# Kernel tuning notes

Hardware: AMD Instinct MI355X
Metric: run time of the kernel (lower is better)

Reference implementation:

```python
import jax, jax.numpy as jnp
import numpy as np

DIM = 256
NUM_HEADS = 8
HEAD_DIM = DIM // NUM_HEADS


def setup_inputs() -> dict:
    key = jax.random.key(0)
    k_x, k_wq, k_bq, k_wp, k_bp = jax.random.split(key, 5)
    B, C, H, W = 2, DIM, 48, 48
    x = jax.random.normal(k_x, (B, C, H, W), dtype=jnp.float32)
    # 1x1 convs are pointwise matmuls: store weights as [out, in]
    w_qkv = jax.random.normal(k_wq, (3 * C, C), dtype=jnp.float32) * (1.0 / np.sqrt(C))
    b_qkv = jax.random.normal(k_bq, (3 * C,), dtype=jnp.float32) * 0.01
    w_proj = jax.random.normal(k_wp, (C, C), dtype=jnp.float32) * (1.0 / np.sqrt(C))
    b_proj = jax.random.normal(k_bp, (C,), dtype=jnp.float32) * 0.01
    return {"x": x, "w_qkv": w_qkv, "b_qkv": b_qkv, "w_proj": w_proj, "b_proj": b_proj}


def reference(x, w_qkv, b_qkv, w_proj, b_proj):
    B, C, H, W = x.shape
    N = H * W
    # qkv 1x1 conv -> pointwise channel matmul
    qkv = jnp.einsum('bchw,oc->bohw', x, w_qkv) + b_qkv[None, :, None, None]
    q, k, v = jnp.split(qkv, 3, axis=1)  # each [B, C, H, W]
    q = q.reshape(B, NUM_HEADS, HEAD_DIM, N)
    k = k.reshape(B, NUM_HEADS, HEAD_DIM, N)
    v = v.reshape(B, NUM_HEADS, HEAD_DIM, N)
    scale = 1.0 / (HEAD_DIM ** 0.5)
    attn = jnp.einsum('bhdn,bhdm->bhnm', q, k) * scale  # [B, H, N, N]
    attn = jax.nn.softmax(attn, axis=-1)
    out = jnp.einsum('bhnm,bhdm->bhdn', attn, v)  # [B, heads, head_dim, N]
    out = out.reshape(B, C, H, W)
    out = jnp.einsum('bchw,oc->bohw', out, w_proj) + b_proj[None, :, None, None]
    return out + x
```

## Files before the change

### kernel.cpp

```cpp
#include <hip/hip_runtime.h>
#include <math.h>

#define C_DIM 256
#define NH 8
#define HD 32
#define BATCH 2
#define NPIX 2304
#define TK 64
#define NGRP (NPIX / 16)
#define TPB 18

typedef __attribute__((ext_vector_type(8))) short bf16x8;
typedef __attribute__((ext_vector_type(4))) float f32x4;

#define OFF_XT  0u
#define OFF_Q   1179648u
#define OFF_K   2359296u
#define OFF_V   3538944u
#define OFF_OT  4718592u
#define OFF_WQ  5898240u
#define OFF_WP  6094848u
#define OFF_F32 6160384u

__device__ __forceinline__ unsigned short f2b(float f) {
    union { float f; unsigned int u; } c; c.f = f;
    unsigned int u = c.u + 0x7FFFu + ((c.u >> 16) & 1u);
    return (unsigned short)(u >> 16);
}
__device__ __forceinline__ unsigned int pk2(float lo, float hi) {
    union { float f; unsigned int u; } a, b;
    a.f = lo; b.f = hi;
    return __builtin_amdgcn_perm(b.u + 0x8000u, a.u + 0x8000u, 0x07060302u);
}

__global__ __launch_bounds__(256) void prep_xt(
        const float* __restrict__ x, unsigned short* __restrict__ xT)
{
    __shared__ unsigned short t_s[64][72];
    const int tid = threadIdx.x;
    const int n0 = blockIdx.x * 64, c0 = blockIdx.y * 64, b = blockIdx.z;
    const int nl = tid & 63, cq = tid >> 6;
    #pragma unroll
    for (int p = 0; p < 8; ++p) {
        const int c = p * 8 + cq * 2;
        const float f0 = x[((size_t)b * C_DIM + c0 + c) * NPIX + n0 + nl];
        const float f1 = x[((size_t)b * C_DIM + c0 + c + 1) * NPIX + n0 + nl];
        *(unsigned int*)&t_s[nl][c] = pk2(f0, f1);
    }
    __syncthreads();
    const int row = tid >> 2, jq = tid & 3;
    #pragma unroll
    for (int hh = 0; hh < 2; ++hh) {
        const int jl = jq * 2 + hh;
        const int jg = blockIdx.y * 8 + jl;
        const int ngrp = blockIdx.x * 4 + (row >> 4);
        unsigned short* dst = xT + (((size_t)b * NGRP + ngrp) * 32 + jg) * 128 + (row & 15) * 8;
        *(uint4*)dst = *(uint4*)&t_s[row][jl * 8];
    }
}

__global__ __launch_bounds__(256) void prep_w(
        const float* __restrict__ wqkv, const float* __restrict__ wproj,
        unsigned short* __restrict__ wq, unsigned short* __restrict__ wp)
{
    const int t = blockIdx.x * 256 + threadIdx.x;
    const float* src; unsigned short* dst;
    if (t < 24576) {
        const int m = t >> 5, j = t & 31;
        src = wqkv + ((size_t)m * C_DIM + j * 8);
        dst = wq + ((size_t)((m >> 4) * 32 + j) * 16 + (m & 15)) * 8;
    } else {
        const int t2 = t - 24576, m = t2 >> 5, j = t2 & 31;
        src = wproj + ((size_t)m * C_DIM + j * 8);
        dst = wp + ((size_t)((m >> 4) * 32 + j) * 16 + (m & 15)) * 8;
    }
    const float4 f0 = *(const float4*)src, f1 = *(const float4*)(src + 4);
    *(uint4*)dst = make_uint4(pk2(f0.x, f0.y), pk2(f0.z, f0.w),
                              pk2(f1.x, f1.y), pk2(f1.z, f1.w));
}

__global__ __launch_bounds__(256, 2) void qkv_gemm(
        const unsigned short* __restrict__ xT, const unsigned short* __restrict__ wq,
        const float* __restrict__ bias,
        unsigned short* __restrict__ Qg, unsigned short* __restrict__ Kg,
        unsigned short* __restrict__ Vg)
{
    __shared__ unsigned short eplds[4][2560];
    const int tid = threadIdx.x, wv = tid >> 6, lane = tid & 63;
    const int l15 = lane & 15, quad = lane >> 4;
    const int n0 = blockIdx.x * 256, my = blockIdx.y, b = blockIdx.z;
    const int nw = n0 + wv * 64;

    bf16x8 af[2][8];
    #pragma unroll
    for (int mt = 0; mt < 2; ++mt)
        #pragma unroll
        for (int kc = 0; kc < 8; ++kc)
            af[mt][kc] = *(const bf16x8*)(wq +
                ((size_t)((my * 2 + mt) * 32 + kc * 4 + quad) * 16 + l15) * 8);

    f32x4 acc[2][4];
    #pragma unroll
    for (int mt = 0; mt < 2; ++mt)
        #pragma unroll
        for (int s = 0; s < 4; ++s) acc[mt][s] = (f32x4){0.f, 0.f, 0.f, 0.f};

    #pragma unroll
    for (int sub = 0; sub < 4; ++sub) {
        const int ngrp = (nw + sub * 16) >> 4;
        const unsigned short* bp = xT + ((size_t)b * NGRP + ngrp) * 32 * 128;
        #pragma unroll
        for (int kc = 0; kc < 8; ++kc) {
            const bf16x8 bf = *(const bf16x8*)(bp + (size_t)(kc * 4 + quad) * 128 + l15 * 8);
            acc[0][sub] = __builtin_amdgcn_mfma_f32_16x16x32_bf16(af[0][kc], bf, acc[0][sub], 0, 0, 0);
            acc[1][sub] = __builtin_amdgcn_mfma_f32_16x16x32_bf16(af[1][kc], bf, acc[1][sub], 0, 0, 0);
        }
    }

    const int which = my >> 3;
    const int h = my & 7, bh = b * NH + h;
    float4 b4[2];
    b4[0] = *(const float4*)(bias + my * 32 + quad * 4);
    b4[1] = *(const float4*)(bias + my * 32 + 16 + quad * 4);
    unsigned short* wl = eplds[wv];

    if (which < 2) {
        const float sc = (which == 0) ? 0.17677669529663687f : 1.0f;
        #pragma unroll
        for (int mt = 0; mt < 2; ++mt)
            #pragma unroll
            for (int sub = 0; sub < 4; ++sub) {
                const float v0 = (acc[mt][sub][0] + b4[mt].x) * sc;
                const float v1 = (acc[mt][sub][1] + b4[mt].y) * sc;
                const float v2 = (acc[mt][sub][2] + b4[mt].z) * sc;
                const float v3 = (acc[mt][sub][3] + b4[mt].w) * sc;
                *(uint2*)&wl[(sub * 16 + l15) * 40 + mt * 16 + quad * 4] =
                    make_uint2(pk2(v0, v1), pk2(v2, v3));
            }
        unsigned short* dst = ((which == 0) ? Qg : Kg)
                            + ((size_t)bh * NPIX + nw + lane) * HD;
        #pragma unroll
        for (int i = 0; i < 4; ++i)
            *((uint4*)dst + i) = *(uint4*)&wl[lane * 40 + i * 8];
    } else {
        #pragma unroll
        for (int mt = 0; mt < 2; ++mt)
            #pragma unroll
            for (int sub = 0; sub < 4; ++sub) {
                wl[(mt * 16 + quad * 4 + 0) * 72 + sub * 16 + l15] = f2b(acc[mt][sub][0] + b4[mt].x);
                wl[(mt * 16 + quad * 4 + 1) * 72 + sub * 16 + l15] = f2b(acc[mt][sub][1] + b4[mt].y);
                wl[(mt * 16 + quad * 4 + 2) * 72 + sub * 16 + l15] = f2b(acc[mt][sub][2] + b4[mt].z);
                wl[(mt * 16 + quad * 4 + 3) * 72 + sub * 16 + l15] = f2b(acc[mt][sub][3] + b4[mt].w);
            }
        const int row = lane >> 1, seg = (lane & 1) * 32;
        unsigned short* dst = Vg + ((size_t)bh * HD + row) * NPIX + nw + seg;
        #pragma unroll
        for (int i = 0; i < 4; ++i)
            *((uint4*)dst + i) = *(uint4*)&wl[row * 72 + seg + i * 8];
    }
}

__global__ __launch_bounds__(256, 4) void attn_kernel(
        const unsigned short* __restrict__ Qg, const unsigned short* __restrict__ Kg,
        const unsigned short* __restrict__ Vg,
        float* __restrict__ OtP, float* __restrict__ lsumP)
{
    __shared__ unsigned short k_s[2][TK][40];
    __shared__ unsigned short v_s[2][HD][76];
    __shared__ unsigned short p_s[4][16][76];

    const int tid  = threadIdx.x;
    const int wv   = tid >> 6;
    const int lane = tid & 63;
    const int l15  = lane & 15;
    const int quad = lane >> 4;
    const int bh   = blockIdx.x;
    const int q0   = blockIdx.y * 64;
    const int sp   = blockIdx.z;
    const int t0   = sp * TPB;

    const unsigned short* Qh = Qg + (size_t)bh * NPIX * HD;
    const unsigned short* Kh = Kg + (size_t)bh * NPIX * HD;
    const unsigned short* Vh = Vg + (size_t)bh * HD * NPIX;

    const bf16x8 q_frag = *(const bf16x8*)(Qh + (size_t)(q0 + wv * 16 + l15) * HD + quad * 8);

    const int kr = tid >> 2, kc = (tid & 3) * 8;
    const int vd = tid >> 3, vc = (tid & 7) * 8;

    uint4 kreg = *(const uint4*)(Kh + (size_t)(t0 * TK + kr) * HD + kc);
    uint4 vreg = *(const uint4*)(Vh + (size_t)vd * NPIX + t0 * TK + vc);
    *(uint4*)&k_s[0][kr][kc] = kreg;
    *(uint4*)&v_s[0][vd][vc] = vreg;

    f32x4 o0 = {0.f, 0.f, 0.f, 0.f};
    f32x4 o1 = {0.f, 0.f, 0.f, 0.f};
    float lsum = 0.f;

    for (int t = 0; t < TPB; ++t) {
        const int cur = t & 1;
        if (t + 1 < TPB) {
            const int k0 = (t0 + t + 1) * TK;
            kreg = *(const uint4*)(Kh + (size_t)(k0 + kr) * HD + kc);
            vreg = *(const uint4*)(Vh + (size_t)vd * NPIX + k0 + vc);
        }
        __syncthreads();

        f32x4 s[4];
        #pragma unroll
        for (int kg = 0; kg < 4; ++kg) {
            const bf16x8 kf = *(const bf16x8*)&k_s[cur][kg * 16 + l15][quad * 8];
            s[kg] = __builtin_amdgcn_mfma_f32_16x16x32_bf16(kf, q_frag,
                        (f32x4){0.f, 0.f, 0.f, 0.f}, 0, 0, 0);
        }

        #pragma unroll
        for (int kg = 0; kg < 4; ++kg) {
            const float p0 = __expf(s[kg][0]);
            const float p1 = __expf(s[kg][1]);
            const float p2 = __expf(s[kg][2]);
            const float p3 = __expf(s[kg][3]);
            lsum += (p0 + p1) + (p2 + p3);
            *(uint2*)&p_s[wv][l15][kg * 16 + quad * 4] =
                make_uint2(pk2(p0, p1), pk2(p2, p3));
        }

        #pragma unroll
        for (int kc2 = 0; kc2 < 2; ++kc2) {
            const bf16x8 pf  = *(const bf16x8*)&p_s[wv][l15][kc2 * 32 + quad * 8];
            const bf16x8 vf0 = *(const bf16x8*)&v_s[cur][l15][kc2 * 32 + quad * 8];
            const bf16x8 vf1 = *(const bf16x8*)&v_s[cur][16 + l15][kc2 * 32 + quad * 8];
            o0 = __builtin_amdgcn_mfma_f32_16x16x32_bf16(vf0, pf, o0, 0, 0, 0);
            o1 = __builtin_amdgcn_mfma_f32_16x16x32_bf16(vf1, pf, o1, 0, 0, 0);
        }

        if (t + 1 < TPB) {
            *(uint4*)&k_s[cur ^ 1][kr][kc] = kreg;
            *(uint4*)&v_s[cur ^ 1][vd][vc] = vreg;
        }
    }

    lsum += __shfl_xor(lsum, 16, 64);
    lsum += __shfl_xor(lsum, 32, 64);

    __syncthreads();
    float* pp = (float*)&p_s[wv][0][0];
    #pragma unroll
    for (int r = 0; r < 4; ++r) {
        pp[l15 * 36 + quad * 4 + r]      = o0[r];
        pp[l15 * 36 + 16 + quad * 4 + r] = o1[r];
    }
    if (quad == 0)
        lsumP[((size_t)sp * 16 + bh) * NPIX + q0 + wv * 16 + l15] = lsum;
    __syncthreads();
    const int q = lane >> 2, off = (lane & 3) * 8;
    float* dst = OtP + (((size_t)sp * 16 + bh) * NPIX + q0 + wv * 16 + q) * 32 + off;
    *(float4*)dst       = *(float4*)&pp[q * 36 + off];
    *((float4*)dst + 1) = *(float4*)&pp[q * 36 + off + 4];
}

__global__ __launch_bounds__(256) void norm_kernel(
        const float* __restrict__ OtP, const float* __restrict__ lsumP,
        unsigned short* __restrict__ OtT)
{
    const int q = blockIdx.x * 256 + threadIdx.x;
    const int bh = blockIdx.y;
    const float* pa = OtP + ((size_t)bh * NPIX + q) * 32;
    const float* pb = OtP + ((size_t)(16 + bh) * NPIX + q) * 32;
    const float inv = 1.f / (lsumP[(size_t)bh * NPIX + q] +
                             lsumP[(size_t)(16 + bh) * NPIX + q]);
    const int b = bh >> 3, h = bh & 7;
    unsigned short* cell = OtT + (((size_t)b * NGRP + (q >> 4)) * 32 + h * 4) * 128
                         + (q & 15) * 8;
    #pragma unroll
    for (int jq = 0; jq < 4; ++jq) {
        const float4 a0 = *(const float4*)(pa + jq * 8);
        const float4 a1 = *(const float4*)(pa + jq * 8 + 4);
        const float4 b0 = *(const float4*)(pb + jq * 8);
        const float4 b1 = *(const float4*)(pb + jq * 8 + 4);
        const float o0 = (a0.x + b0.x) * inv, o1 = (a0.y + b0.y) * inv;
        const float o2 = (a0.z + b0.z) * inv, o3 = (a0.w + b0.w) * inv;
        const float o4 = (a1.x + b1.x) * inv, o5 = (a1.y + b1.y) * inv;
        const float o6 = (a1.z + b1.z) * inv, o7 = (a1.w + b1.w) * inv;
        *(uint4*)(cell + jq * 128) = make_uint4(pk2(o0, o1), pk2(o2, o3),
                                                pk2(o4, o5), pk2(o6, o7));
    }
}

__global__ __launch_bounds__(256) void proj_gemm(
        const unsigned short* __restrict__ OtT, const unsigned short* __restrict__ wp,
        const float* __restrict__ bias, const float* __restrict__ x,
        float* __restrict__ out)
{
    __shared__ float plds[4][576];
    const int tid = threadIdx.x, wv = tid >> 6, lane = tid & 63;
    const int l15 = lane & 15, quad = lane >> 4;
    const int n0 = blockIdx.x * 128, my = blockIdx.y, b = blockIdx.z;
    const int nw = n0 + wv * 32;

    bf16x8 af[8];
    #pragma unroll
    for (int kc = 0; kc < 8; ++kc)
        af[kc] = *(const bf16x8*)(wp + ((size_t)(my * 32 + kc * 4 + quad) * 16 + l15) * 8);

    f32x4 acc[2];
    acc[0] = (f32x4){0.f, 0.f, 0.f, 0.f};
    acc[1] = (f32x4){0.f, 0.f, 0.f, 0.f};

    #pragma unroll
    for (int sub = 0; sub < 2; ++sub) {
        const int ngrp = (nw + sub * 16) >> 4;
        const unsigned short* bp = OtT + ((size_t)b * NGRP + ngrp) * 32 * 128;
        #pragma unroll
        for (int kc = 0; kc < 8; ++kc) {
            const bf16x8 bf = *(const bf16x8*)(bp + (size_t)(kc * 4 + quad) * 128 + l15 * 8);
            acc[sub] = __builtin_amdgcn_mfma_f32_16x16x32_bf16(af[kc], bf, acc[sub], 0, 0, 0);
        }
    }

    float* wl = plds[wv];
    #pragma unroll
    for (int sub = 0; sub < 2; ++sub) {
        wl[(quad * 4 + 0) * 36 + sub * 16 + l15] = acc[sub][0];
        wl[(quad * 4 + 1) * 36 + sub * 16 + l15] = acc[sub][1];
        wl[(quad * 4 + 2) * 36 + sub * 16 + l15] = acc[sub][2];
        wl[(quad * 4 + 3) * 36 + sub * 16 + l15] = acc[sub][3];
    }
    const int m0 = my * 16;
    #pragma unroll
    for (int p = 0; p < 2; ++p) {
        const int row = p * 8 + (lane >> 3), cn = (lane & 7) * 4;
        const int c = m0 + row;
        const size_t idx = ((size_t)b * C_DIM + c) * NPIX + nw + cn;
        const f32x4 v = *(const f32x4*)&wl[row * 36 + cn];
        const f32x4 r = *(const f32x4*)(x + idx);
        const float bv = bias[c];
        f32x4 o;
        o[0] = v[0] + bv + r[0]; o[1] = v[1] + bv + r[1];
        o[2] = v[2] + bv + r[2]; o[3] = v[3] + bv + r[3];
        *(f32x4*)(out + idx) = o;
    }
}

extern "C" void kernel_launch(void* const* d_in, const int* in_sizes, int n_in,
                              void* d_out, int out_size, void* d_ws, size_t ws_size,
                              hipStream_t stream)
{
    const float* x      = (const float*)d_in[0];
    const float* w_qkv  = (const float*)d_in[1];
    const float* b_qkv  = (const float*)d_in[2];
    const float* w_proj = (const float*)d_in[3];
    const float* b_proj = (const float*)d_in[4];
    float* out = (float*)d_out;

    unsigned short* ws = (unsigned short*)d_ws;
    unsigned short* xT  = ws + OFF_XT;
    unsigned short* Qg  = ws + OFF_Q;
    unsigned short* Kg  = ws + OFF_K;
    unsigned short* Vg  = ws + OFF_V;
    unsigned short* OtT = ws + OFF_OT;
    unsigned short* wq  = ws + OFF_WQ;
    unsigned short* wp  = ws + OFF_WP;
    float* fws   = (float*)(ws + OFF_F32);
    float* OtP   = fws;
    float* lsumP = fws + 4718592;

    prep_xt<<<dim3(36, 4, 2), 256, 0, stream>>>(x, xT);
    prep_w<<<dim3(128), 256, 0, stream>>>(w_qkv, w_proj, wq, wp);
    qkv_gemm<<<dim3(9, 24, 2), 256, 0, stream>>>(xT, wq, b_qkv, Qg, Kg, Vg);
    attn_kernel<<<dim3(16, 36, 2), 256, 0, stream>>>(Qg, Kg, Vg, OtP, lsumP);
    norm_kernel<<<dim3(9, 16), 256, 0, stream>>>(OtP, lsumP, OtT);
    proj_gemm<<<dim3(18, 16, 2), 256, 0, stream>>>(OtT, wp, b_proj, x, out);
}
```

Baseline: 117.3 us.

## Use exp2 with folded log2e scale, MFMA row sums, hardware bf16 pack

```diff
diff --git a/kernel.cpp b/kernel.cpp
--- a/kernel.cpp
+++ b/kernel.cpp
@@ -31,6 +31,18 @@
     union { float f; unsigned int u; } a, b;
     a.f = lo; b.f = hi;
     return __builtin_amdgcn_perm(b.u + 0x8000u, a.u + 0x8000u, 0x07060302u);
+}
+__device__ __forceinline__ unsigned int cvtpk(float lo, float hi) {
+    unsigned int r;
+    asm("v_cvt_pk_bf16_f32 %0, %1, %2" : "=v"(r) : "v"(lo), "v"(hi));
+    return r;
+}
+__device__ __forceinline__ float fexp2(float x) {
+#if __has_builtin(__builtin_amdgcn_exp2f)
+    return __builtin_amdgcn_exp2f(x);
+#else
+    return exp2f(x);
+#endif
 }
 
 __global__ __launch_bounds__(256) void prep_xt(
@@ -125,7 +137,7 @@
     unsigned short* wl = eplds[wv];
 
     if (which < 2) {
-        const float sc = (which == 0) ? 0.17677669529663687f : 1.0f;
+        const float sc = (which == 0) ? 0.2550348576f : 1.0f;
         #pragma unroll
         for (int mt = 0; mt < 2; ++mt)
             #pragma unroll
@@ -184,6 +196,7 @@
     const unsigned short* Vh = Vg + (size_t)bh * HD * NPIX;
 
     const bf16x8 q_frag = *(const bf16x8*)(Qh + (size_t)(q0 + wv * 16 + l15) * HD + quad * 8);
+    const bf16x8 onesf = {16256, 16256, 16256, 16256, 16256, 16256, 16256, 16256};
 
     const int kr = tid >> 2, kc = (tid & 3) * 8;
     const int vd = tid >> 3, vc = (tid & 7) * 8;
@@ -195,7 +208,7 @@
 
     f32x4 o0 = {0.f, 0.f, 0.f, 0.f};
     f32x4 o1 = {0.f, 0.f, 0.f, 0.f};
-    float lsum = 0.f;
+    f32x4 ol = {0.f, 0.f, 0.f, 0.f};
 
     for (int t = 0; t < TPB; ++t) {
         const int cur = t & 1;
@@ -216,13 +229,12 @@
 
         #pragma unroll
         for (int kg = 0; kg < 4; ++kg) {
-            const float p0 = __expf(s[kg][0]);
-            const float p1 = __expf(s[kg][1]);
-            const float p2 = __expf(s[kg][2]);
-            const float p3 = __expf(s[kg][3]);
-            lsum += (p0 + p1) + (p2 + p3);
+            const float p0 = fexp2(s[kg][0]);
+            const float p1 = fexp2(s[kg][1]);
+            const float p2 = fexp2(s[kg][2]);
+            const float p3 = fexp2(s[kg][3]);
             *(uint2*)&p_s[wv][l15][kg * 16 + quad * 4] =
-                make_uint2(pk2(p0, p1), pk2(p2, p3));
+                make_uint2(cvtpk(p0, p1), cvtpk(p2, p3));
         }
 
         #pragma unroll
@@ -232,6 +244,7 @@
             const bf16x8 vf1 = *(const bf16x8*)&v_s[cur][16 + l15][kc2 * 32 + quad * 8];
             o0 = __builtin_amdgcn_mfma_f32_16x16x32_bf16(vf0, pf, o0, 0, 0, 0);
             o1 = __builtin_amdgcn_mfma_f32_16x16x32_bf16(vf1, pf, o1, 0, 0, 0);
+            ol = __builtin_amdgcn_mfma_f32_16x16x32_bf16(onesf, pf, ol, 0, 0, 0);
         }
 
         if (t + 1 < TPB) {
@@ -240,9 +253,6 @@
         }
     }
 
-    lsum += __shfl_xor(lsum, 16, 64);
-    lsum += __shfl_xor(lsum, 32, 64);
-
     __syncthreads();
     float* pp = (float*)&p_s[wv][0][0];
     #pragma unroll
@@ -251,7 +261,7 @@
         pp[l15 * 36 + 16 + quad * 4 + r] = o1[r];
     }
     if (quad == 0)
-        lsumP[((size_t)sp * 16 + bh) * NPIX + q0 + wv * 16 + l15] = lsum;
+        lsumP[((size_t)sp * 16 + bh) * NPIX + q0 + wv * 16 + l15] = ol[0];
     __syncthreads();
     const int q = lane >> 2, off = (lane & 3) * 8;
     float* dst = OtP + (((size_t)sp * 16 + bh) * NPIX + q0 + wv * 16 + q) * 32 + off;
@@ -263,28 +273,26 @@
         const float* __restrict__ OtP, const float* __restrict__ lsumP,
         unsigned short* __restrict__ OtT)
 {
-    const int q = blockIdx.x * 256 + threadIdx.x;
+    const int t = blockIdx.x * 256 + threadIdx.x;
+    const int q = t >> 2, jq = t & 3;
     const int bh = blockIdx.y;
-    const float* pa = OtP + ((size_t)bh * NPIX + q) * 32;
-    const float* pb = OtP + ((size_t)(16 + bh) * NPIX + q) * 32;
+    const float* pa = OtP + ((size_t)bh * NPIX + q) * 32 + jq * 8;
+    const float* pb = OtP + ((size_t)(16 + bh) * NPIX + q) * 32 + jq * 8;
     const float inv = 1.f / (lsumP[(size_t)bh * NPIX + q] +
                              lsumP[(size_t)(16 + bh) * NPIX + q]);
     const int b = bh >> 3, h = bh & 7;
     unsigned short* cell = OtT + (((size_t)b * NGRP + (q >> 4)) * 32 + h * 4) * 128
-                         + (q & 15) * 8;
-    #pragma unroll
-    for (int jq = 0; jq < 4; ++jq) {
-        const float4 a0 = *(const float4*)(pa + jq * 8);
-        const float4 a1 = *(const float4*)(pa + jq * 8 + 4);
-        const float4 b0 = *(const float4*)(pb + jq * 8);
-        const float4 b1 = *(const float4*)(pb + jq * 8 + 4);
-        const float o0 = (a0.x + b0.x) * inv, o1 = (a0.y + b0.y) * inv;
-        const float o2 = (a0.z + b0.z) * inv, o3 = (a0.w + b0.w) * inv;
-        const float o4 = (a1.x + b1.x) * inv, o5 = (a1.y + b1.y) * inv;
-        const float o6 = (a1.z + b1.z) * inv, o7 = (a1.w + b1.w) * inv;
-        *(uint4*)(cell + jq * 128) = make_uint4(pk2(o0, o1), pk2(o2, o3),
-                                                pk2(o4, o5), pk2(o6, o7));
-    }
+                         + (q & 15) * 8 + jq * 128;
+    const float4 a0 = *(const float4*)(pa);
+    const float4 a1 = *(const float4*)(pa + 4);
+    const float4 b0 = *(const float4*)(pb);
+    const float4 b1 = *(const float4*)(pb + 4);
+    const float o0 = (a0.x + b0.x) * inv, o1 = (a0.y + b0.y) * inv;
+    const float o2 = (a0.z + b0.z) * inv, o3 = (a0.w + b0.w) * inv;
+    const float o4 = (a1.x + b1.x) * inv, o5 = (a1.y + b1.y) * inv;
+    const float o6 = (a1.z + b1.z) * inv, o7 = (a1.w + b1.w) * inv;
+    *(uint4*)cell = make_uint4(cvtpk(o0, o1), cvtpk(o2, o3),
+                               cvtpk(o4, o5), cvtpk(o6, o7));
 }
 
 __global__ __launch_bounds__(256) void proj_gemm(
@@ -369,6 +377,6 @@
     prep_w<<<dim3(128), 256, 0, stream>>>(w_qkv, w_proj, wq, wp);
     qkv_gemm<<<dim3(9, 24, 2), 256, 0, stream>>>(xT, wq, b_qkv, Qg, Kg, Vg);
     attn_kernel<<<dim3(16, 36, 2), 256, 0, stream>>>(Qg, Kg, Vg, OtP, lsumP);
-    norm_kernel<<<dim3(9, 16), 256, 0, stream>>>(OtP, lsumP, OtT);
+    norm_kernel<<<dim3(36, 16), 256, 0, stream>>>(OtP, lsumP, OtT);
     proj_gemm<<<dim3(18, 16, 2), 256, 0, stream>>>(OtT, wp, b_proj, x, out);
 }
```

Result: faster. 114.7 us (-2.2%).
